# Kernel tuning notes

Measured on AMD Instinct MI355X. Metric: run time of the kernel, lower is better.

Reference implementation:

```python
import jax, jax.numpy as jnp
import numpy as np

VOCAB = 339503
D = 200            # embbeding_dim == hidden_dim
B, S, W = 64, 128, 32   # batch, max segments per sample, words per segment
T, WL = 128, 32         # law segments, words per law segment


def setup_inputs() -> dict:
    key = jax.random.key(0)
    ks = jax.random.split(key, 8)
    text_ids = jax.random.randint(ks[0], (B, S, W), 0, VOCAB)
    text_lens = jax.random.randint(ks[1], (B,), 1, S + 1)  # >=1 valid segment
    law_ids = jax.random.randint(ks[2], (T, WL), 0, VOCAB)
    emb_table = jax.random.normal(ks[3], (VOCAB, D), jnp.float32) * 0.02
    W1 = jax.random.normal(ks[4], (2 * D, 2 * D), jnp.float32) * 0.05
    b1 = jnp.zeros((2 * D,), jnp.float32)
    W2 = jax.random.normal(ks[5], (2 * D, 6), jnp.float32) * 0.05
    b2 = jnp.zeros((6,), jnp.float32)
    return dict(text_ids=text_ids, text_lens=text_lens, law_ids=law_ids,
                emb_table=emb_table, W1=W1, b1=b1, W2=W2, b2=b2)


def _forward(text_ids, text_lens, law_ids, emb_table, W1, b1, W2, b2):
    # encoder: embedding gather + mean over words, zero-pad invalid segments
    text_emb = emb_table[text_ids].mean(axis=2)                 # [B,S,D]
    seg_mask = jnp.arange(S)[None, :] < text_lens[:, None]      # [B,S]
    text_emb = text_emb * seg_mask[:, :, None]
    law_emb = emb_table[law_ids].mean(axis=1)                   # [T,D]
    law_rep = jnp.broadcast_to(law_emb[None], (text_ids.shape[0], T, D))

    # AoA: attention-over-attention between fact segments and law segments
    M = jnp.einsum('bsd,btd->bst', text_emb, law_rep)           # [B,S,T]
    neg = jnp.finfo(M.dtype).min
    alpha = jax.nn.softmax(M, axis=2)                           # over law dim (full length)
    beta = jax.nn.softmax(jnp.where(seg_mask[:, :, None], M, neg), axis=1)  # over fact dim, masked
    avg_alpha = alpha.mean(axis=2, keepdims=True)               # [B,S,1]
    avg_beta = beta.mean(axis=1)[:, :, None]                    # [B,T,1]

    # RSABlock: residual scale + mean-pool + concat
    fact = (text_emb + text_emb * avg_alpha).mean(axis=1)       # [B,D]
    label = (law_rep + law_rep * avg_beta).mean(axis=1)         # [B,D]
    feat = jnp.concatenate([fact, label], axis=-1)              # [B,2D]

    # deep FC head + softmax
    h = jax.nn.relu(feat @ W1 + b1)
    predict = jax.nn.softmax(h @ W2 + b2, axis=1)               # [B,6]
    return predict, avg_alpha


def reference(text_ids, text_lens, law_ids, emb_table, W1, b1, W2, b2):
    return _forward(text_ids, text_lens, law_ids, emb_table, W1, b1, W2, b2)
```

## Files before the change

### kernel.cpp

```cpp
#include <hip/hip_runtime.h>

namespace {
constexpr int B   = 64;
constexpr int S   = 128;
constexpr int Wd  = 32;
constexpr int T   = 128;
constexpr int D   = 200;
constexpr int SEGS = 4;
constexpr int CHB  = S / SEGS;
constexpr int CHL  = T / SEGS;
constexpr int NTXT = B * CHB;
constexpr float CC = (129.0f / 128.0f) / 4096.0f;
using f32x4 = __attribute__((ext_vector_type(4))) float;
}

__global__ void gather_sum_kernel(const int* __restrict__ text_ids,
                                  const int* __restrict__ text_lens,
                                  const int* __restrict__ law_ids,
                                  const float* __restrict__ emb,
                                  float* __restrict__ fact_part,
                                  float* __restrict__ law_part) {
  __shared__ int ids[SEGS * Wd];
  __shared__ __align__(16) float wsum[4][D];
  const int tid = threadIdx.x;
  const int blk = blockIdx.x;
  const bool isLaw = (blk >= NTXT);
  const int b = blk / CHB;
  const int chunk = blk % CHB;

  if (!isLaw) {
    const int len = text_lens[b];
    if (chunk * SEGS >= len) {
      if (tid < D) fact_part[(size_t)blk * D + tid] = 0.f;
      return;
    }
    if (tid < SEGS * Wd) {
      const int s = chunk * SEGS + (tid >> 5);
      ids[tid] = (s < len) ? text_ids[((size_t)b * S + s) * Wd + (tid & 31)] : -1;
    }
  } else {
    if (tid < SEGS * Wd) ids[tid] = law_ids[(size_t)(blk - NTXT) * (SEGS * Wd) + tid];
  }
  __syncthreads();

  const int w = tid >> 6;
  const int lane = tid & 63;
  const f32x4* __restrict__ embv = reinterpret_cast<const f32x4*>(emb);
  if (lane < 50) {
    f32x4 a0 = 0.f, a1 = 0.f, a2 = 0.f, a3 = 0.f;
    #pragma unroll
    for (int r = 0; r < 32; r += 4) {
      const int i0 = ids[w * 32 + r + 0];
      const int i1 = ids[w * 32 + r + 1];
      const int i2 = ids[w * 32 + r + 2];
      const int i3 = ids[w * 32 + r + 3];
      const float m0 = (i0 >= 0) ? 1.f : 0.f;
      const float m1 = (i1 >= 0) ? 1.f : 0.f;
      const float m2 = (i2 >= 0) ? 1.f : 0.f;
      const float m3 = (i3 >= 0) ? 1.f : 0.f;
      const size_t r0 = (size_t)(i0 >= 0 ? i0 : 0) * 50 + lane;
      const size_t r1 = (size_t)(i1 >= 0 ? i1 : 0) * 50 + lane;
      const size_t r2 = (size_t)(i2 >= 0 ? i2 : 0) * 50 + lane;
      const size_t r3 = (size_t)(i3 >= 0 ? i3 : 0) * 50 + lane;
      a0 += embv[r0] * m0;
      a1 += embv[r1] * m1;
      a2 += embv[r2] * m2;
      a3 += embv[r3] * m3;
    }
    *reinterpret_cast<f32x4*>(&wsum[w][lane * 4]) = (a0 + a1) + (a2 + a3);
  }
  __syncthreads();

  if (tid < D) {
    const float rv = (wsum[0][tid] + wsum[1][tid]) + (wsum[2][tid] + wsum[3][tid]);
    if (isLaw) law_part[(size_t)(blk - NTXT) * D + tid] = rv;
    else       fact_part[(size_t)blk * D + tid] = rv;
  }
}

__global__ void gemv_part_kernel(const float* __restrict__ fact_part,
                                 const float* __restrict__ law_part,
                                 const float* __restrict__ W1,
                                 float* __restrict__ hpart) {
  __shared__ float red[4][100];
  __shared__ float featq[100];
  const int bq = blockIdx.x;
  const int b = bq >> 2;
  const int q = bq & 3;
  const int tid = threadIdx.x;

  if (tid < 400) {
    const int il = tid % 100;
    const int kg = tid / 100;
    const int ig = q * 100 + il;
    const float* p = (ig < 2 * D / 2)
        ? fact_part + ((size_t)b * CHB + kg * 8) * D + ig
        : law_part + (size_t)(kg * 8) * D + (ig - D);
    float s = 0.f;
    #pragma unroll
    for (int k = 0; k < 8; ++k) s += p[(size_t)k * D];
    red[kg][il] = s;
  }
  __syncthreads();
  if (tid < 100)
    featq[tid] = ((red[0][tid] + red[1][tid]) + (red[2][tid] + red[3][tid])) * CC;
  __syncthreads();

  if (tid < 400) {
    const float* Wp = W1 + (size_t)(q * 100) * 400 + tid;
    float c0 = 0.f, c1 = 0.f, c2 = 0.f, c3 = 0.f;
    #pragma unroll
    for (int i = 0; i < 100; i += 4) {
      c0 = fmaf(featq[i + 0], Wp[(size_t)(i + 0) * 400], c0);
      c1 = fmaf(featq[i + 1], Wp[(size_t)(i + 1) * 400], c1);
      c2 = fmaf(featq[i + 2], Wp[(size_t)(i + 2) * 400], c2);
      c3 = fmaf(featq[i + 3], Wp[(size_t)(i + 3) * 400], c3);
    }
    hpart[(size_t)bq * 400 + tid] = (c0 + c1) + (c2 + c3);
  }
}

__global__ void finish_kernel(const float* __restrict__ hpart,
                              const float* __restrict__ b1,
                              const float* __restrict__ W2,
                              const float* __restrict__ b2,
                              float* __restrict__ out) {
  __shared__ float h[400];
  __shared__ float logits[6];
  const int b = blockIdx.x;
  const int tid = threadIdx.x;

  if (tid < S) out[B * 6 + b * S + tid] = 1.0f / 128.0f;

  if (tid < 400) {
    const float* p = hpart + (size_t)b * 4 * 400 + tid;
    const float v = b1[tid] + ((p[0] + p[400]) + (p[800] + p[1200]));
    h[tid] = fmaxf(v, 0.f);
  }
  __syncthreads();

  if (tid < 6 * 64) {
    const int k = tid >> 6;
    const int lane = tid & 63;
    float acc = 0.f;
    for (int j = lane; j < 400; j += 64) acc = fmaf(h[j], W2[(size_t)j * 6 + k], acc);
    #pragma unroll
    for (int off = 32; off; off >>= 1) acc += __shfl_down(acc, off);
    if (lane == 0) logits[k] = acc + b2[k];
  }
  __syncthreads();

  if (tid == 0) {
    float m = logits[0];
    for (int k = 1; k < 6; ++k) m = fmaxf(m, logits[k]);
    float e[6], ssum = 0.f;
    for (int k = 0; k < 6; ++k) { e[k] = expf(logits[k] - m); ssum += e[k]; }
    const float inv = 1.0f / ssum;
    for (int k = 0; k < 6; ++k) out[b * 6 + k] = e[k] * inv;
  }
}

extern "C" void kernel_launch(void* const* d_in, const int* in_sizes, int n_in,
                              void* d_out, int out_size, void* d_ws, size_t ws_size,
                              hipStream_t stream) {
  const int*   text_ids  = (const int*)d_in[0];
  const int*   text_lens = (const int*)d_in[1];
  const int*   law_ids   = (const int*)d_in[2];
  const float* emb       = (const float*)d_in[3];
  const float* W1        = (const float*)d_in[4];
  const float* b1        = (const float*)d_in[5];
  const float* W2        = (const float*)d_in[6];
  const float* b2        = (const float*)d_in[7];
  float* out = (float*)d_out;

  float* fact_part = (float*)d_ws;
  float* law_part  = fact_part + (size_t)NTXT * D;
  float* hpart     = law_part + (size_t)CHL * D;

  hipLaunchKernelGGL(gather_sum_kernel, dim3(NTXT + CHL), dim3(256), 0, stream,
                     text_ids, text_lens, law_ids, emb, fact_part, law_part);
  hipLaunchKernelGGL(gemv_part_kernel, dim3(B * 4), dim3(512), 0, stream,
                     fact_part, law_part, W1, hpart);
  hipLaunchKernelGGL(finish_kernel, dim3(B), dim3(512), 0, stream,
                     hpart, b1, W2, b2, out);
}
```

Before: 35.89 us.

## Fuse FC head into one kernel and halve segments per gather block

Merges the partial GEMV kernel and the finish kernel into a single head kernel. Each of the 64 blocks now reduces the fact and law partial sums, runs the full 400x400 W1 GEMV, then applies the W2 layer and softmax, which removes one launch and the hpart round trip through global memory. The gather kernel now handles 2 segments per block instead of 4, doubling the block count, and uses 8 independent accumulators per wave to keep more loads in flight. The trade-off is that each head block does a 400-step serial GEMV over all of W1 with only 64 blocks, instead of splitting it into four 100-row pieces across 256 blocks, so the head stage has less parallelism.

Result: slower. 37.54 us (+4.6%).

```diff
diff --git a/kernel.cpp b/kernel.cpp
--- a/kernel.cpp
+++ b/kernel.cpp
@@ -6,10 +6,11 @@
 constexpr int Wd  = 32;
 constexpr int T   = 128;
 constexpr int D   = 200;
-constexpr int SEGS = 4;
+constexpr int SEGS = 2;
 constexpr int CHB  = S / SEGS;
 constexpr int CHL  = T / SEGS;
 constexpr int NTXT = B * CHB;
+constexpr int ROWS = SEGS * Wd;
 constexpr float CC = (129.0f / 128.0f) / 4096.0f;
 using f32x4 = __attribute__((ext_vector_type(4))) float;
 }
@@ -20,26 +21,26 @@
                                   const float* __restrict__ emb,
                                   float* __restrict__ fact_part,
                                   float* __restrict__ law_part) {
-  __shared__ int ids[SEGS * Wd];
+  __shared__ int ids[ROWS];
   __shared__ __align__(16) float wsum[4][D];
   const int tid = threadIdx.x;
   const int blk = blockIdx.x;
   const bool isLaw = (blk >= NTXT);
-  const int b = blk / CHB;
-  const int chunk = blk % CHB;
 
   if (!isLaw) {
+    const int b = blk >> 6;
+    const int chunk = blk & 63;
     const int len = text_lens[b];
     if (chunk * SEGS >= len) {
       if (tid < D) fact_part[(size_t)blk * D + tid] = 0.f;
       return;
     }
-    if (tid < SEGS * Wd) {
+    if (tid < ROWS) {
       const int s = chunk * SEGS + (tid >> 5);
       ids[tid] = (s < len) ? text_ids[((size_t)b * S + s) * Wd + (tid & 31)] : -1;
     }
   } else {
-    if (tid < SEGS * Wd) ids[tid] = law_ids[(size_t)(blk - NTXT) * (SEGS * Wd) + tid];
+    if (tid < ROWS) ids[tid] = law_ids[(size_t)(blk - NTXT) * ROWS + tid];
   }
   __syncthreads();
 
@@ -48,26 +49,28 @@
   const f32x4* __restrict__ embv = reinterpret_cast<const f32x4*>(emb);
   if (lane < 50) {
     f32x4 a0 = 0.f, a1 = 0.f, a2 = 0.f, a3 = 0.f;
+    f32x4 a4 = 0.f, a5 = 0.f, a6 = 0.f, a7 = 0.f;
     #pragma unroll
-    for (int r = 0; r < 32; r += 4) {
-      const int i0 = ids[w * 32 + r + 0];
-      const int i1 = ids[w * 32 + r + 1];
-      const int i2 = ids[w * 32 + r + 2];
-      const int i3 = ids[w * 32 + r + 3];
-      const float m0 = (i0 >= 0) ? 1.f : 0.f;
-      const float m1 = (i1 >= 0) ? 1.f : 0.f;
-      const float m2 = (i2 >= 0) ? 1.f : 0.f;
-      const float m3 = (i3 >= 0) ? 1.f : 0.f;
-      const size_t r0 = (size_t)(i0 >= 0 ? i0 : 0) * 50 + lane;
-      const size_t r1 = (size_t)(i1 >= 0 ? i1 : 0) * 50 + lane;
-      const size_t r2 = (size_t)(i2 >= 0 ? i2 : 0) * 50 + lane;
-      const size_t r3 = (size_t)(i3 >= 0 ? i3 : 0) * 50 + lane;
-      a0 += embv[r0] * m0;
-      a1 += embv[r1] * m1;
-      a2 += embv[r2] * m2;
-      a3 += embv[r3] * m3;
+    for (int r = 0; r < 16; r += 8) {
+      const int i0 = ids[w * 16 + r + 0];
+      const int i1 = ids[w * 16 + r + 1];
+      const int i2 = ids[w * 16 + r + 2];
+      const int i3 = ids[w * 16 + r + 3];
+      const int i4 = ids[w * 16 + r + 4];
+      const int i5 = ids[w * 16 + r + 5];
+      const int i6 = ids[w * 16 + r + 6];
+      const int i7 = ids[w * 16 + r + 7];
+      a0 += embv[(size_t)(i0 >= 0 ? i0 : 0) * 50 + lane] * (i0 >= 0 ? 1.f : 0.f);
+      a1 += embv[(size_t)(i1 >= 0 ? i1 : 0) * 50 + lane] * (i1 >= 0 ? 1.f : 0.f);
+      a2 += embv[(size_t)(i2 >= 0 ? i2 : 0) * 50 + lane] * (i2 >= 0 ? 1.f : 0.f);
+      a3 += embv[(size_t)(i3 >= 0 ? i3 : 0) * 50 + lane] * (i3 >= 0 ? 1.f : 0.f);
+      a4 += embv[(size_t)(i4 >= 0 ? i4 : 0) * 50 + lane] * (i4 >= 0 ? 1.f : 0.f);
+      a5 += embv[(size_t)(i5 >= 0 ? i5 : 0) * 50 + lane] * (i5 >= 0 ? 1.f : 0.f);
+      a6 += embv[(size_t)(i6 >= 0 ? i6 : 0) * 50 + lane] * (i6 >= 0 ? 1.f : 0.f);
+      a7 += embv[(size_t)(i7 >= 0 ? i7 : 0) * 50 + lane] * (i7 >= 0 ? 1.f : 0.f);
     }
-    *reinterpret_cast<f32x4*>(&wsum[w][lane * 4]) = (a0 + a1) + (a2 + a3);
+    const f32x4 s = ((a0 + a1) + (a2 + a3)) + ((a4 + a5) + (a6 + a7));
+    *reinterpret_cast<f32x4*>(&wsum[w][lane * 4]) = s;
   }
   __syncthreads();
 
@@ -78,64 +81,58 @@
   }
 }
 
-__global__ void gemv_part_kernel(const float* __restrict__ fact_part,
-                                 const float* __restrict__ law_part,
-                                 const float* __restrict__ W1,
-                                 float* __restrict__ hpart) {
-  __shared__ float red[4][100];
-  __shared__ float featq[100];
-  const int bq = blockIdx.x;
-  const int b = bq >> 2;
-  const int q = bq & 3;
-  const int tid = threadIdx.x;
-
-  if (tid < 400) {
-    const int il = tid % 100;
-    const int kg = tid / 100;
-    const int ig = q * 100 + il;
-    const float* p = (ig < 2 * D / 2)
-        ? fact_part + ((size_t)b * CHB + kg * 8) * D + ig
-        : law_part + (size_t)(kg * 8) * D + (ig - D);
-    float s = 0.f;
-    #pragma unroll
-    for (int k = 0; k < 8; ++k) s += p[(size_t)k * D];
-    red[kg][il] = s;
-  }
-  __syncthreads();
-  if (tid < 100)
-    featq[tid] = ((red[0][tid] + red[1][tid]) + (red[2][tid] + red[3][tid])) * CC;
-  __syncthreads();
-
-  if (tid < 400) {
-    const float* Wp = W1 + (size_t)(q * 100) * 400 + tid;
-    float c0 = 0.f, c1 = 0.f, c2 = 0.f, c3 = 0.f;
-    #pragma unroll
-    for (int i = 0; i < 100; i += 4) {
-      c0 = fmaf(featq[i + 0], Wp[(size_t)(i + 0) * 400], c0);
-      c1 = fmaf(featq[i + 1], Wp[(size_t)(i + 1) * 400], c1);
-      c2 = fmaf(featq[i + 2], Wp[(size_t)(i + 2) * 400], c2);
-      c3 = fmaf(featq[i + 3], Wp[(size_t)(i + 3) * 400], c3);
-    }
-    hpart[(size_t)bq * 400 + tid] = (c0 + c1) + (c2 + c3);
-  }
-}
-
-__global__ void finish_kernel(const float* __restrict__ hpart,
-                              const float* __restrict__ b1,
-                              const float* __restrict__ W2,
-                              const float* __restrict__ b2,
-                              float* __restrict__ out) {
-  __shared__ float h[400];
+__global__ __launch_bounds__(512) void head_kernel(
+    const float* __restrict__ fact_part,
+    const float* __restrict__ law_part,
+    const float* __restrict__ W1,
+    const float* __restrict__ b1,
+    const float* __restrict__ W2,
+    const float* __restrict__ b2,
+    float* __restrict__ out) {
+  __shared__ float feat[2 * D];
+  __shared__ float h[2 * D];
   __shared__ float logits[6];
   const int b = blockIdx.x;
   const int tid = threadIdx.x;
 
   if (tid < S) out[B * 6 + b * S + tid] = 1.0f / 128.0f;
 
-  if (tid < 400) {
-    const float* p = hpart + (size_t)b * 4 * 400 + tid;
-    const float v = b1[tid] + ((p[0] + p[400]) + (p[800] + p[1200]));
-    h[tid] = fmaxf(v, 0.f);
+  if (tid < D) {
+    const float* p = fact_part + (size_t)b * CHB * D + tid;
+    float s0 = 0.f, s1 = 0.f, s2 = 0.f, s3 = 0.f;
+    #pragma unroll
+    for (int k = 0; k < CHB; k += 4) {
+      s0 += p[(size_t)(k + 0) * D];
+      s1 += p[(size_t)(k + 1) * D];
+      s2 += p[(size_t)(k + 2) * D];
+      s3 += p[(size_t)(k + 3) * D];
+    }
+    feat[tid] = ((s0 + s1) + (s2 + s3)) * CC;
+  } else if (tid >= 256 && tid < 256 + D) {
+    const int d = tid - 256;
+    const float* p = law_part + d;
+    float s0 = 0.f, s1 = 0.f, s2 = 0.f, s3 = 0.f;
+    #pragma unroll
+    for (int k = 0; k < CHL; k += 4) {
+      s0 += p[(size_t)(k + 0) * D];
+      s1 += p[(size_t)(k + 1) * D];
+      s2 += p[(size_t)(k + 2) * D];
+      s3 += p[(size_t)(k + 3) * D];
+    }
+    feat[D + d] = ((s0 + s1) + (s2 + s3)) * CC;
+  }
+  __syncthreads();
+
+  if (tid < 2 * D) {
+    const float* Wp = W1 + tid;
+    float c0 = b1[tid], c1 = 0.f, c2 = 0.f, c3 = 0.f;
+    for (int i = 0; i < 2 * D; i += 4) {
+      c0 = fmaf(feat[i + 0], Wp[(size_t)(i + 0) * 400], c0);
+      c1 = fmaf(feat[i + 1], Wp[(size_t)(i + 1) * 400], c1);
+      c2 = fmaf(feat[i + 2], Wp[(size_t)(i + 2) * 400], c2);
+      c3 = fmaf(feat[i + 3], Wp[(size_t)(i + 3) * 400], c3);
+    }
+    h[tid] = fmaxf((c0 + c1) + (c2 + c3), 0.f);
   }
   __syncthreads();
 
@@ -143,7 +140,7 @@
     const int k = tid >> 6;
     const int lane = tid & 63;
     float acc = 0.f;
-    for (int j = lane; j < 400; j += 64) acc = fmaf(h[j], W2[(size_t)j * 6 + k], acc);
+    for (int j = lane; j < 2 * D; j += 64) acc = fmaf(h[j], W2[(size_t)j * 6 + k], acc);
     #pragma unroll
     for (int off = 32; off; off >>= 1) acc += __shfl_down(acc, off);
     if (lane == 0) logits[k] = acc + b2[k];
@@ -175,12 +172,9 @@
 
   float* fact_part = (float*)d_ws;
   float* law_part  = fact_part + (size_t)NTXT * D;
-  float* hpart     = law_part + (size_t)CHL * D;
 
   hipLaunchKernelGGL(gather_sum_kernel, dim3(NTXT + CHL), dim3(256), 0, stream,
                      text_ids, text_lens, law_ids, emb, fact_part, law_part);
-  hipLaunchKernelGGL(gemv_part_kernel, dim3(B * 4), dim3(512), 0, stream,
-                     fact_part, law_part, W1, hpart);
-  hipLaunchKernelGGL(finish_kernel, dim3(B), dim3(512), 0, stream,
-                     hpart, b1, W2, b2, out);
+  hipLaunchKernelGGL(head_kernel, dim3(B), dim3(512), 0, stream,
+                     fact_part, law_part, W1, b1, W2, b2, out);
 }
```
